# Kernel optimization log

Hardware: AMD Instinct MI355X
Metric: run time of the kernel (lower is better)

## Reference

```python
import jax, jax.numpy as jnp
import numpy as np

B = 64


def _upsample_conv1x1(f, cw, cb, size):
    # bilinear upsample (align_corners=False == jax half-pixel) + 1x1 conv
    u = jax.image.resize(f, (f.shape[0], f.shape[1], size, size), method='bilinear')
    return jnp.einsum('bchw,oc->bohw', u, cw) + cb[None, :, None, None]


def _shuffle_byblock(x, perms, block_size):
    # Rearrange 'b c (h h1) (w w1) -> b c (h w) h1 w1', then per-block channel
    # permutation: shuffled[:, j, i] = blocks[:, perms[i, j], i], then inverse.
    Bsz, C, H, _ = x.shape
    nb = H // block_size
    blocks = x.reshape(Bsz, C, nb, block_size, nb, block_size)
    blocks = blocks.transpose(0, 1, 2, 4, 3, 5).reshape(Bsz, C, nb * nb, block_size, block_size)
    idx = perms[: nb * nb].T  # [C, nb*nb]; idx[j, i] = perms[i, j]
    shuf = jnp.take_along_axis(blocks, idx[None, :, :, None, None], axis=1)
    shuf = shuf.reshape(Bsz, C, nb, nb, block_size, block_size)
    shuf = shuf.transpose(0, 1, 2, 4, 3, 5).reshape(Bsz, C, H, H)
    return shuf


def setup_inputs() -> dict:
    key = jax.random.key(0)
    ks = jax.random.split(key, 10)
    f1 = jax.random.normal(ks[0], (B, 64, 28, 28), jnp.float32)
    f2 = jax.random.normal(ks[1], (B, 128, 14, 14), jnp.float32)
    f3 = jax.random.normal(ks[2], (B, 128, 7, 7), jnp.float32)
    f4 = jax.random.normal(ks[3], (B, 512, 7, 7), jnp.float32)
    x_final = jax.random.normal(ks[4], (B, 512), jnp.float32)
    cw1 = jax.random.normal(ks[5], (64, 64), jnp.float32) * 0.1
    cb1 = jnp.zeros((64,), jnp.float32)
    cw2 = jax.random.normal(ks[6], (128, 128), jnp.float32) * 0.1
    cb2 = jnp.zeros((128,), jnp.float32)
    cw3 = jax.random.normal(ks[7], (256, 128), jnp.float32) * 0.1
    cb3 = jnp.zeros((256,), jnp.float32)
    cw4 = jax.random.normal(ks[8], (512, 512), jnp.float32) * 0.1
    cb4 = jnp.zeros((512,), jnp.float32)
    w1 = jnp.ones((64, 56, 56), jnp.float32)
    w2 = jnp.ones((128, 28, 28), jnp.float32)
    w3 = jnp.ones((256, 14, 14), jnp.float32)
    w4 = jnp.ones((512, 7, 7), jnp.float32)
    rng = np.random.default_rng(0)
    perms = jnp.asarray(np.stack([rng.permutation(64) for _ in range(28 * 28)]).astype(np.int32))
    return dict(f1=f1, f2=f2, f3=f3, f4=f4, x_final=x_final,
                cw1=cw1, cb1=cb1, cw2=cw2, cb2=cb2, cw3=cw3, cb3=cb3, cw4=cw4, cb4=cb4,
                w1=w1, w2=w2, w3=w3, w4=w4, perms=perms)


def reference(f1, f2, f3, f4, x_final, cw1, cb1, cw2, cb2, cw3, cb3, cw4, cb4,
              w1, w2, w3, w4, perms):
    aux1 = _shuffle_byblock(_upsample_conv1x1(f1, cw1, cb1, 56), perms, 28)
    aux2 = _upsample_conv1x1(f2, cw2, cb2, 28)
    aux3 = _upsample_conv1x1(f3, cw3, cb3, 14)
    aux4 = _upsample_conv1x1(f4, cw4, cb4, 7)
    return (x_final, aux1, aux2, aux3, aux4, w1, w2, w3, w4)
```

## Files before the change

kernel.cpp:

```cpp
#include <hip/hip_runtime.h>
#include <hip/hip_bf16.h>
#include <cstddef>

typedef __attribute__((ext_vector_type(8))) short bf16x8;
typedef __attribute__((ext_vector_type(4))) float f32x4;

__device__ __forceinline__ float4 ld4(const float* p) { return *(const float4*)p; }
__device__ __forceinline__ unsigned short f2bf(float v) {
  __hip_bfloat16 h = __float2bfloat16(v);
  return *(unsigned short*)&h;
}

__device__ __forceinline__ bf16x8 pack8(float v0, float v1, float v2, float v3,
                                        float v4, float v5, float v6, float v7) {
  bf16x8 r;
  r[0] = (short)f2bf(v0); r[1] = (short)f2bf(v1);
  r[2] = (short)f2bf(v2); r[3] = (short)f2bf(v3);
  r[4] = (short)f2bf(v4); r[5] = (short)f2bf(v5);
  r[6] = (short)f2bf(v6); r[7] = (short)f2bf(v7);
  return r;
}
__device__ __forceinline__ bf16x8 cfrag(const float* __restrict__ p) {
  float4 a = ld4(p), b = ld4(p + 4);
  return pack8(a.x, a.y, a.z, a.w, b.x, b.y, b.z, b.w);
}
__device__ __forceinline__ bf16x8 gfrag(const float* __restrict__ p, int stride) {
  float v0 = p[0], v1 = p[stride], v2 = p[2 * stride], v3 = p[3 * stride];
  float v4 = p[4 * stride], v5 = p[5 * stride], v6 = p[6 * stride], v7 = p[7 * stride];
  return pack8(v0, v1, v2, v3, v4, v5, v6, v7);
}
__device__ __forceinline__ bf16x8 gfrag_guard(const float* __restrict__ p, int stride, bool ok) {
  float v0 = ok ? p[0] : 0.f, v1 = ok ? p[stride] : 0.f;
  float v2 = ok ? p[2 * stride] : 0.f, v3 = ok ? p[3 * stride] : 0.f;
  float v4 = ok ? p[4 * stride] : 0.f, v5 = ok ? p[5 * stride] : 0.f;
  float v6 = ok ? p[6 * stride] : 0.f, v7 = ok ? p[7 * stride] : 0.f;
  return pack8(v0, v1, v2, v3, v4, v5, v6, v7);
}

__device__ __forceinline__ void up_quad_rows(const float* __restrict__ s0,
                                             const float* __restrict__ s1,
                                             const float* __restrict__ s2,
                                             int qx, int W, float* __restrict__ dst, int pitch) {
  int cm = qx > 0 ? qx - 1 : 0, cp = qx < W - 1 ? qx + 1 : W - 1;
  float tA0 = 0.25f * s0[cm] + 0.75f * s0[qx], tA1 = 0.75f * s0[qx] + 0.25f * s0[cp];
  float tB0 = 0.25f * s1[cm] + 0.75f * s1[qx], tB1 = 0.75f * s1[qx] + 0.25f * s1[cp];
  float tC0 = 0.25f * s2[cm] + 0.75f * s2[qx], tC1 = 0.75f * s2[qx] + 0.25f * s2[cp];
  *(float2*)dst = make_float2(0.25f * tA0 + 0.75f * tB0, 0.25f * tA1 + 0.75f * tB1);
  *(float2*)(dst + pitch) = make_float2(0.75f * tB0 + 0.25f * tC0, 0.75f * tB1 + 0.25f * tC1);
}

__device__ __forceinline__ void up_quad2(const float* __restrict__ s0,
                                         const float* __restrict__ s1,
                                         const float* __restrict__ s2,
                                         int qx0, int W, float* __restrict__ dst, int pitch) {
  int cm = qx0 > 0 ? qx0 - 1 : 0;
  int c2 = qx0 + 2 < W ? qx0 + 2 : W - 1;
  float Am = s0[cm], A0 = s0[qx0], A1 = s0[qx0 + 1], A2 = s0[c2];
  float Bm = s1[cm], B0 = s1[qx0], B1 = s1[qx0 + 1], B2 = s1[c2];
  float Cm = s2[cm], C0 = s2[qx0], C1 = s2[qx0 + 1], C2 = s2[c2];
  float hA0 = 0.25f * Am + 0.75f * A0, hA1 = 0.75f * A0 + 0.25f * A1;
  float hA2 = 0.25f * A0 + 0.75f * A1, hA3 = 0.75f * A1 + 0.25f * A2;
  float hB0 = 0.25f * Bm + 0.75f * B0, hB1 = 0.75f * B0 + 0.25f * B1;
  float hB2 = 0.25f * B0 + 0.75f * B1, hB3 = 0.75f * B1 + 0.25f * B2;
  float hC0 = 0.25f * Cm + 0.75f * C0, hC1 = 0.75f * C0 + 0.25f * C1;
  float hC2 = 0.25f * C0 + 0.75f * C1, hC3 = 0.75f * C1 + 0.25f * C2;
  *(float4*)dst = make_float4(0.25f * hA0 + 0.75f * hB0, 0.25f * hA1 + 0.75f * hB1,
                              0.25f * hA2 + 0.75f * hB2, 0.25f * hA3 + 0.75f * hB3);
  *(float4*)(dst + pitch) = make_float4(0.75f * hB0 + 0.25f * hC0, 0.75f * hB1 + 0.25f * hC1,
                                        0.75f * hB2 + 0.25f * hC2, 0.75f * hB3 + 0.25f * hC3);
}

struct P1M { float ct[16][252]; int inv[4][16]; };
struct C2M { float ct[32][126]; };
struct C3M { float ct[64][49]; };
union SmemM { P1M p1; C2M c2; C3M c3; };

__device__ __forceinline__ int2 xcd_decode(int d, int wpb_log) {
  int xcd = d & 7;
  int i = (d >> 3) & ((1 << wpb_log) - 1);
  int b = (((d >> (3 + wpb_log)) << 3) | xcd);
  return make_int2(b, i);
}

__global__ void __launch_bounds__(256)
fused_all(const float* __restrict__ f1, const float* __restrict__ f2,
          const float* __restrict__ f3, const float* __restrict__ f4,
          const float* __restrict__ cw1, const float* __restrict__ cb1,
          const float* __restrict__ cw2, const float* __restrict__ cb2,
          const float* __restrict__ cw3, const float* __restrict__ cb3,
          const float* __restrict__ cw4, const float* __restrict__ cb4,
          const float* __restrict__ xf, const float* __restrict__ w1,
          const float* __restrict__ w2, const float* __restrict__ w3,
          const float* __restrict__ w4s, const int* __restrict__ perms,
          float* __restrict__ out) {
  __shared__ SmemM sm;
  const int raw = blockIdx.x, tid = threadIdx.x;
  const int wave = tid >> 6, lane = tid & 63;
  const int l15 = lane & 15, lg = lane >> 4;
  float* o_aux1 = out + 32768;
  float* o_aux2 = o_aux1 + 12845056;
  float* o_aux3 = o_aux2 + 6422528;
  float* o_aux4 = o_aux3 + 3211264;

  if (raw < 128) {
    int2 bi = xcd_decode(raw, 1);
    const int b = bi.x;
    const int ob = bi.y * 256 + wave * 64;
    const float* f4b = f4 + (size_t)b * 25088;

    f32x4 acc[4][4];
#pragma unroll
    for (int mi = 0; mi < 4; ++mi) {
      float bv0 = cb4[ob + mi * 16 + lg * 4 + 0], bv1 = cb4[ob + mi * 16 + lg * 4 + 1];
      float bv2 = cb4[ob + mi * 16 + lg * 4 + 2], bv3 = cb4[ob + mi * 16 + lg * 4 + 3];
#pragma unroll
      for (int n = 0; n < 4; ++n) {
        acc[mi][n][0] = bv0; acc[mi][n][1] = bv1; acc[mi][n][2] = bv2; acc[mi][n][3] = bv3;
      }
    }
    int poff[4]; bool pok[4];
#pragma unroll
    for (int n = 0; n < 4; ++n) {
      int p = n * 16 + l15;
      pok[n] = p < 49;
      poff[n] = pok[n] ? p : 0;
    }
#pragma unroll 1
    for (int k0 = 0; k0 < 512; k0 += 32) {
      bf16x8 A0 = cfrag(cw4 + (size_t)(ob + 0 + l15) * 512 + k0 + lg * 8);
      bf16x8 A1 = cfrag(cw4 + (size_t)(ob + 16 + l15) * 512 + k0 + lg * 8);
      bf16x8 A2 = cfrag(cw4 + (size_t)(ob + 32 + l15) * 512 + k0 + lg * 8);
      bf16x8 A3 = cfrag(cw4 + (size_t)(ob + 48 + l15) * 512 + k0 + lg * 8);
      const float* fb = f4b + (size_t)(k0 + lg * 8) * 49;
      bf16x8 B0 = gfrag_guard(fb + poff[0], 49, pok[0]);
      bf16x8 B1 = gfrag_guard(fb + poff[1], 49, pok[1]);
      bf16x8 B2 = gfrag_guard(fb + poff[2], 49, pok[2]);
      bf16x8 B3 = gfrag_guard(fb + poff[3], 49, pok[3]);
      acc[0][0] = __builtin_amdgcn_mfma_f32_16x16x32_bf16(A0, B0, acc[0][0], 0, 0, 0);
      acc[0][1] = __builtin_amdgcn_mfma_f32_16x16x32_bf16(A0, B1, acc[0][1], 0, 0, 0);
      acc[0][2] = __builtin_amdgcn_mfma_f32_16x16x32_bf16(A0, B2, acc[0][2], 0, 0, 0);
      acc[0][3] = __builtin_amdgcn_mfma_f32_16x16x32_bf16(A0, B3, acc[0][3], 0, 0, 0);
      acc[1][0] = __builtin_amdgcn_mfma_f32_16x16x32_bf16(A1, B0, acc[1][0], 0, 0, 0);
      acc[1][1] = __builtin_amdgcn_mfma_f32_16x16x32_bf16(A1, B1, acc[1][1], 0, 0, 0);
      acc[1][2] = __builtin_amdgcn_mfma_f32_16x16x32_bf16(A1, B2, acc[1][2], 0, 0, 0);
      acc[1][3] = __builtin_amdgcn_mfma_f32_16x16x32_bf16(A1, B3, acc[1][3], 0, 0, 0);
      acc[2][0] = __builtin_amdgcn_mfma_f32_16x16x32_bf16(A2, B0, acc[2][0], 0, 0, 0);
      acc[2][1] = __builtin_amdgcn_mfma_f32_16x16x32_bf16(A2, B1, acc[2][1], 0, 0, 0);
      acc[2][2] = __builtin_amdgcn_mfma_f32_16x16x32_bf16(A2, B2, acc[2][2], 0, 0, 0);
      acc[2][3] = __builtin_amdgcn_mfma_f32_16x16x32_bf16(A2, B3, acc[2][3], 0, 0, 0);
      acc[3][0] = __builtin_amdgcn_mfma_f32_16x16x32_bf16(A3, B0, acc[3][0], 0, 0, 0);
      acc[3][1] = __builtin_amdgcn_mfma_f32_16x16x32_bf16(A3, B1, acc[3][1], 0, 0, 0);
      acc[3][2] = __builtin_amdgcn_mfma_f32_16x16x32_bf16(A3, B2, acc[3][2], 0, 0, 0);
      acc[3][3] = __builtin_amdgcn_mfma_f32_16x16x32_bf16(A3, B3, acc[3][3], 0, 0, 0);
    }
    float* outb = o_aux4 + (size_t)b * 25088;
#pragma unroll
    for (int mi = 0; mi < 4; ++mi) {
#pragma unroll
      for (int n = 0; n < 4; ++n) {
        int p = n * 16 + l15;
        if (p < 49) {
#pragma unroll
          for (int r = 0; r < 4; ++r) {
            int o = ob + mi * 16 + lg * 4 + r;
            outb[(size_t)o * 49 + p] = acc[mi][n][r];
          }
        }
      }
    }
  } else if (raw < 1152) {
    int2 bi = xcd_decode(raw - 128, 4);
    const int b = bi.x;
    const int o0 = (bi.y >> 2) * 16;
    const int r0 = (bi.y & 3) * 7, base = r0 - 1;
    const float* f1b = f1 + (size_t)b * 50176;

    if (tid >= 128 && tid < 192) {
      int t2 = tid - 128;
      int i = t2 >> 4, cl = t2 & 15;
      int c = o0 + cl;
      int r = 0;
      for (int j = 0; j < 64; ++j)
        if (perms[i * 64 + j] == c) r = j;
      sm.p1.inv[i][cl] = r;
    }

    int off[4];
#pragma unroll
    for (int j = 0; j < 4; ++j) {
      int praw = wave * 64 + j * 16 + l15;
      int p = praw < 251 ? praw : 251;
      int lr = p / 28, x = p - lr * 28;
      int sr = base + lr;
      sr = sr < 0 ? 0 : (sr > 27 ? 27 : sr);
      off[j] = sr * 28 + x;
    }
    f32x4 acc[4];
    {
      float bv0 = cb1[o0 + lg * 4 + 0], bv1 = cb1[o0 + lg * 4 + 1];
      float bv2 = cb1[o0 + lg * 4 + 2], bv3 = cb1[o0 + lg * 4 + 3];
#pragma unroll
      for (int j = 0; j < 4; ++j) {
        acc[j][0] = bv0; acc[j][1] = bv1; acc[j][2] = bv2; acc[j][3] = bv3;
      }
    }
    const float* ap = cw1 + (size_t)(o0 + l15) * 64 + lg * 8;
#pragma unroll
    for (int ks = 0; ks < 2; ++ks) {
      bf16x8 A = cfrag(ap + ks * 32);
      const float* fb = f1b + (size_t)(ks * 32 + lg * 8) * 784;
#pragma unroll
      for (int j = 0; j < 4; ++j) {
        bf16x8 B = gfrag(fb + off[j], 784);
        acc[j] = __builtin_amdgcn_mfma_f32_16x16x32_bf16(A, B, acc[j], 0, 0, 0);
      }
    }
#pragma unroll
    for (int j = 0; j < 4; ++j) {
      int praw = wave * 64 + j * 16 + l15;
      if (praw < 252) {
#pragma unroll
        for (int r = 0; r < 4; ++r) sm.p1.ct[lg * 4 + r][praw] = acc[j][r];
      }
    }
    __syncthreads();

    const size_t obase = (size_t)b * 200704;
    for (int i = tid; i < 1568; i += 256) {
      int cl = i / 98;
      int rem = i - cl * 98;
      int ly = rem / 14, pr = rem - ly * 14;
      int qx0 = 2 * pr;
      int qy = r0 + ly;
      int lr = ly + 1;
      int qi = ((qy >= 14) ? 2 : 0) + ((qx0 >= 14) ? 1 : 0);
      int j = sm.p1.inv[qi][cl];
      float* dst = o_aux1 + obase + (size_t)j * 3136 + (size_t)(2 * qy) * 56 + 2 * qx0;
      up_quad2(&sm.p1.ct[cl][(lr - 1) * 28], &sm.p1.ct[cl][lr * 28],
               &sm.p1.ct[cl][(lr + 1) * 28], qx0, 28, dst, 56);
    }
  } else if (raw < 1664) {
    int2 bi = xcd_decode(raw - 1152, 3);
    const int b = bi.x;
    const int o0 = (bi.y >> 1) * 32;
    const int r0 = (bi.y & 1) * 7, base = r0 - 1;
    const int og = wave >> 1, nt = wave & 1;
    const int om = o0 + og * 16;
    const float* f2b = f2 + (size_t)b * 25088;

    int off[4];
#pragma unroll
    for (int j = 0; j < 4; ++j) {
      int praw = nt * 64 + j * 16 + l15;
      int p = praw < 125 ? praw : 125;
      int lr = p / 14, x = p - lr * 14;
      int sr = base + lr;
      sr = sr < 0 ? 0 : (sr > 13 ? 13 : sr);
      off[j] = sr * 14 + x;
    }
    f32x4 acc[4];
    {
      float bv0 = cb2[om + lg * 4 + 0], bv1 = cb2[om + lg * 4 + 1];
      float bv2 = cb2[om + lg * 4 + 2], bv3 = cb2[om + lg * 4 + 3];
#pragma unroll
      for (int j = 0; j < 4; ++j) {
        acc[j][0] = bv0; acc[j][1] = bv1; acc[j][2] = bv2; acc[j][3] = bv3;
      }
    }
    const float* ap = cw2 + (size_t)(om + l15) * 128 + lg * 8;
#pragma unroll
    for (int ks = 0; ks < 4; ++ks) {
      bf16x8 A = cfrag(ap + ks * 32);
      const float* fb = f2b + (size_t)(ks * 32 + lg * 8) * 196;
#pragma unroll
      for (int j = 0; j < 4; ++j) {
        bf16x8 B = gfrag(fb + off[j], 196);
        acc[j] = __builtin_amdgcn_mfma_f32_16x16x32_bf16(A, B, acc[j], 0, 0, 0);
      }
    }
#pragma unroll
    for (int j = 0; j < 4; ++j) {
      int praw = nt * 64 + j * 16 + l15;
      if (praw < 126) {
#pragma unroll
        for (int r = 0; r < 4; ++r) sm.c2.ct[og * 16 + lg * 4 + r][praw] = acc[j][r];
      }
    }
    __syncthreads();

    const size_t obase = (size_t)b * 100352;
    for (int i = tid; i < 1568; i += 256) {
      int cl = i / 49;
      int rem = i - cl * 49;
      int ly = rem / 7, pr = rem - ly * 7;
      int qx0 = 2 * pr;
      int qy = r0 + ly;
      int lr = ly + 1;
      float* dst = o_aux2 + obase + (size_t)(o0 + cl) * 784 + (size_t)(2 * qy) * 28 + 2 * qx0;
      up_quad2(&sm.c2.ct[cl][(lr - 1) * 14], &sm.c2.ct[cl][lr * 14],
               &sm.c2.ct[cl][(lr + 1) * 14], qx0, 14, dst, 28);
    }
  } else if (raw < 1920) {
    int2 bi = xcd_decode(raw - 1664, 2);
    const int b = bi.x;
    const int o0 = bi.y * 64;
    const int om = o0 + wave * 16;
    const float* f3b = f3 + (size_t)b * 6272;

    int poff[4]; bool pok[4];
#pragma unroll
    for (int j = 0; j < 4; ++j) {
      int p = j * 16 + l15;
      pok[j] = p < 49;
      poff[j] = pok[j] ? p : 0;
    }
    f32x4 acc[4];
    {
      float bv0 = cb3[om + lg * 4 + 0], bv1 = cb3[om + lg * 4 + 1];
      float bv2 = cb3[om + lg * 4 + 2], bv3 = cb3[om + lg * 4 + 3];
#pragma unroll
      for (int j = 0; j < 4; ++j) {
        acc[j][0] = bv0; acc[j][1] = bv1; acc[j][2] = bv2; acc[j][3] = bv3;
      }
    }
    const float* ap = cw3 + (size_t)(om + l15) * 128 + lg * 8;
#pragma unroll
    for (int ks = 0; ks < 4; ++ks) {
      bf16x8 A = cfrag(ap + ks * 32);
      const float* fb = f3b + (size_t)(ks * 32 + lg * 8) * 49;
#pragma unroll
      for (int j = 0; j < 4; ++j) {
        bf16x8 B = gfrag_guard(fb + poff[j], 49, pok[j]);
        acc[j] = __builtin_amdgcn_mfma_f32_16x16x32_bf16(A, B, acc[j], 0, 0, 0);
      }
    }
#pragma unroll
    for (int j = 0; j < 4; ++j) {
      int p = j * 16 + l15;
      if (p < 49) {
#pragma unroll
        for (int r = 0; r < 4; ++r) sm.c3.ct[wave * 16 + lg * 4 + r][p] = acc[j][r];
      }
    }
    __syncthreads();

    const size_t obase = (size_t)b * 50176;
    for (int i = tid; i < 64 * 49; i += 256) {
      int cl = i / 49;
      int q = i - cl * 49;
      int qy = q / 7, qx = q - qy * 7;
      int rm = qy > 0 ? qy - 1 : 0, rp = qy < 6 ? qy + 1 : 6;
      float* dst = o_aux3 + obase + (size_t)(o0 + cl) * 196 + (size_t)(2 * qy) * 14 + 2 * qx;
      up_quad_rows(&sm.c3.ct[cl][rm * 7], &sm.c3.ct[cl][qy * 7], &sm.c3.ct[cl][rp * 7],
                   qx, 7, dst, 14);
    }
  } else {
    int idx = (raw - 1920) * 256 + tid;
    const int stride = 64 * 256;
    float4* o4 = (float4*)out;
    const size_t W1 = 6029312;
    for (int i = idx; i < 8192; i += stride) o4[i] = ((const float4*)xf)[i];
    for (int i = idx; i < 50176; i += stride) o4[W1 + i] = ((const float4*)w1)[i];
    for (int i = idx; i < 25088; i += stride) o4[W1 + 50176 + i] = ((const float4*)w2)[i];
    for (int i = idx; i < 12544; i += stride) o4[W1 + 75264 + i] = ((const float4*)w3)[i];
    for (int i = idx; i < 6272; i += stride) o4[W1 + 87808 + i] = ((const float4*)w4s)[i];
  }
}

extern "C" void kernel_launch(void* const* d_in, const int* in_sizes, int n_in,
                              void* d_out, int out_size, void* d_ws, size_t ws_size,
                              hipStream_t stream) {
  const float* f1      = (const float*)d_in[0];
  const float* f2      = (const float*)d_in[1];
  const float* f3      = (const float*)d_in[2];
  const float* f4      = (const float*)d_in[3];
  const float* x_final = (const float*)d_in[4];
  const float* cw1     = (const float*)d_in[5];
  const float* cb1     = (const float*)d_in[6];
  const float* cw2     = (const float*)d_in[7];
  const float* cb2     = (const float*)d_in[8];
  const float* cw3     = (const float*)d_in[9];
  const float* cb3     = (const float*)d_in[10];
  const float* cw4     = (const float*)d_in[11];
  const float* cb4     = (const float*)d_in[12];
  const float* w1      = (const float*)d_in[13];
  const float* w2      = (const float*)d_in[14];
  const float* w3      = (const float*)d_in[15];
  const float* w4      = (const float*)d_in[16];
  const int*   perms   = (const int*)d_in[17];

  float* out = (float*)d_out;

  fused_all<<<1984, 256, 0, stream>>>(f1, f2, f3, f4, cw1, cb1, cw2, cb2,
                                      cw3, cb3, cw4, cb4, x_final, w1, w2, w3, w4,
                                      perms, out);
}
```

Before: 48.92 us.

## Interleave all task types per batch in block index ordering

Replaces the segmented block mapping, where each output head occupied a contiguous range of block ids, with a per-batch grouping. Each group of 31 slots per XCD holds 16 aux1, 8 aux2, 4 aux3, 2 aux4 and 1 copy block for the same batch element. The aim is to mix heavy and light block types across the dispatch order so that CUs stay balanced and all work for one batch lands on the same XCD, improving L2 locality. The grid total of 1984 blocks is unchanged, so the scheme relies on the launch count matching 64*31.

```diff
diff --git a/kernel.cpp b/kernel.cpp
--- a/kernel.cpp
+++ b/kernel.cpp
@@ -75,13 +75,6 @@
 struct C3M { float ct[64][49]; };
 union SmemM { P1M p1; C2M c2; C3M c3; };
 
-__device__ __forceinline__ int2 xcd_decode(int d, int wpb_log) {
-  int xcd = d & 7;
-  int i = (d >> 3) & ((1 << wpb_log) - 1);
-  int b = (((d >> (3 + wpb_log)) << 3) | xcd);
-  return make_int2(b, i);
-}
-
 __global__ void __launch_bounds__(256)
 fused_all(const float* __restrict__ f1, const float* __restrict__ f2,
           const float* __restrict__ f3, const float* __restrict__ f4,
@@ -94,7 +87,12 @@
           const float* __restrict__ w4s, const int* __restrict__ perms,
           float* __restrict__ out) {
   __shared__ SmemM sm;
-  const int raw = blockIdx.x, tid = threadIdx.x;
+  const int d = blockIdx.x, tid = threadIdx.x;
+  const int xcd = d & 7;
+  const int slot = d >> 3;
+  const int g = slot / 31;
+  const int r = slot - g * 31;
+  const int b = g * 8 + xcd;
   const int wave = tid >> 6, lane = tid & 63;
   const int l15 = lane & 15, lg = lane >> 4;
   float* o_aux1 = out + 32768;
@@ -102,10 +100,192 @@
   float* o_aux3 = o_aux2 + 6422528;
   float* o_aux4 = o_aux3 + 3211264;
 
-  if (raw < 128) {
-    int2 bi = xcd_decode(raw, 1);
-    const int b = bi.x;
-    const int ob = bi.y * 256 + wave * 64;
+  if (r < 16) {
+    const int i = r;
+    const int o0 = (i >> 2) * 16;
+    const int r0 = (i & 3) * 7, base = r0 - 1;
+    const float* f1b = f1 + (size_t)b * 50176;
+
+    if (tid >= 128 && tid < 192) {
+      int t2 = tid - 128;
+      int qi = t2 >> 4, cl = t2 & 15;
+      int c = o0 + cl;
+      int rr = 0;
+      for (int j = 0; j < 64; ++j)
+        if (perms[qi * 64 + j] == c) rr = j;
+      sm.p1.inv[qi][cl] = rr;
+    }
+
+    int off[4];
+#pragma unroll
+    for (int j = 0; j < 4; ++j) {
+      int praw = wave * 64 + j * 16 + l15;
+      int p = praw < 251 ? praw : 251;
+      int lr = p / 28, x = p - lr * 28;
+      int sr = base + lr;
+      sr = sr < 0 ? 0 : (sr > 27 ? 27 : sr);
+      off[j] = sr * 28 + x;
+    }
+    f32x4 acc[4];
+    {
+      float bv0 = cb1[o0 + lg * 4 + 0], bv1 = cb1[o0 + lg * 4 + 1];
+      float bv2 = cb1[o0 + lg * 4 + 2], bv3 = cb1[o0 + lg * 4 + 3];
+#pragma unroll
+      for (int j = 0; j < 4; ++j) {
+        acc[j][0] = bv0; acc[j][1] = bv1; acc[j][2] = bv2; acc[j][3] = bv3;
+      }
+    }
+    const float* ap = cw1 + (size_t)(o0 + l15) * 64 + lg * 8;
+#pragma unroll
+    for (int ks = 0; ks < 2; ++ks) {
+      bf16x8 A = cfrag(ap + ks * 32);
+      const float* fb = f1b + (size_t)(ks * 32 + lg * 8) * 784;
+#pragma unroll
+      for (int j = 0; j < 4; ++j) {
+        bf16x8 B = gfrag(fb + off[j], 784);
+        acc[j] = __builtin_amdgcn_mfma_f32_16x16x32_bf16(A, B, acc[j], 0, 0, 0);
+      }
+    }
+#pragma unroll
+    for (int j = 0; j < 4; ++j) {
+      int praw = wave * 64 + j * 16 + l15;
+      if (praw < 252) {
+#pragma unroll
+        for (int rr = 0; rr < 4; ++rr) sm.p1.ct[lg * 4 + rr][praw] = acc[j][rr];
+      }
+    }
+    __syncthreads();
+
+    const size_t obase = (size_t)b * 200704;
+    for (int i2 = tid; i2 < 1568; i2 += 256) {
+      int cl = i2 / 98;
+      int rem = i2 - cl * 98;
+      int ly = rem / 14, pr = rem - ly * 14;
+      int qx0 = 2 * pr;
+      int qy = r0 + ly;
+      int lr = ly + 1;
+      int qi = ((qy >= 14) ? 2 : 0) + ((qx0 >= 14) ? 1 : 0);
+      int j = sm.p1.inv[qi][cl];
+      float* dst = o_aux1 + obase + (size_t)j * 3136 + (size_t)(2 * qy) * 56 + 2 * qx0;
+      up_quad2(&sm.p1.ct[cl][(lr - 1) * 28], &sm.p1.ct[cl][lr * 28],
+               &sm.p1.ct[cl][(lr + 1) * 28], qx0, 28, dst, 56);
+    }
+  } else if (r < 24) {
+    const int i = r - 16;
+    const int o0 = (i >> 1) * 32;
+    const int r0 = (i & 1) * 7, base = r0 - 1;
+    const int og = wave >> 1, nt = wave & 1;
+    const int om = o0 + og * 16;
+    const float* f2b = f2 + (size_t)b * 25088;
+
+    int off[4];
+#pragma unroll
+    for (int j = 0; j < 4; ++j) {
+      int praw = nt * 64 + j * 16 + l15;
+      int p = praw < 125 ? praw : 125;
+      int lr = p / 14, x = p - lr * 14;
+      int sr = base + lr;
+      sr = sr < 0 ? 0 : (sr > 13 ? 13 : sr);
+      off[j] = sr * 14 + x;
+    }
+    f32x4 acc[4];
+    {
+      float bv0 = cb2[om + lg * 4 + 0], bv1 = cb2[om + lg * 4 + 1];
+      float bv2 = cb2[om + lg * 4 + 2], bv3 = cb2[om + lg * 4 + 3];
+#pragma unroll
+      for (int j = 0; j < 4; ++j) {
+        acc[j][0] = bv0; acc[j][1] = bv1; acc[j][2] = bv2; acc[j][3] = bv3;
+      }
+    }
+    const float* ap = cw2 + (size_t)(om + l15) * 128 + lg * 8;
+#pragma unroll
+    for (int ks = 0; ks < 4; ++ks) {
+      bf16x8 A = cfrag(ap + ks * 32);
+      const float* fb = f2b + (size_t)(ks * 32 + lg * 8) * 196;
+#pragma unroll
+      for (int j = 0; j < 4; ++j) {
+        bf16x8 B = gfrag(fb + off[j], 196);
+        acc[j] = __builtin_amdgcn_mfma_f32_16x16x32_bf16(A, B, acc[j], 0, 0, 0);
+      }
+    }
+#pragma unroll
+    for (int j = 0; j < 4; ++j) {
+      int praw = nt * 64 + j * 16 + l15;
+      if (praw < 126) {
+#pragma unroll
+        for (int rr = 0; rr < 4; ++rr) sm.c2.ct[og * 16 + lg * 4 + rr][praw] = acc[j][rr];
+      }
+    }
+    __syncthreads();
+
+    const size_t obase = (size_t)b * 100352;
+    for (int i2 = tid; i2 < 1568; i2 += 256) {
+      int cl = i2 / 49;
+      int rem = i2 - cl * 49;
+      int ly = rem / 7, pr = rem - ly * 7;
+      int qx0 = 2 * pr;
+      int qy = r0 + ly;
+      int lr = ly + 1;
+      float* dst = o_aux2 + obase + (size_t)(o0 + cl) * 784 + (size_t)(2 * qy) * 28 + 2 * qx0;
+      up_quad2(&sm.c2.ct[cl][(lr - 1) * 14], &sm.c2.ct[cl][lr * 14],
+               &sm.c2.ct[cl][(lr + 1) * 14], qx0, 14, dst, 28);
+    }
+  } else if (r < 28) {
+    const int i = r - 24;
+    const int o0 = i * 64;
+    const int om = o0 + wave * 16;
+    const float* f3b = f3 + (size_t)b * 6272;
+
+    int poff[4]; bool pok[4];
+#pragma unroll
+    for (int j = 0; j < 4; ++j) {
+      int p = j * 16 + l15;
+      pok[j] = p < 49;
+      poff[j] = pok[j] ? p : 0;
+    }
+    f32x4 acc[4];
+    {
+      float bv0 = cb3[om + lg * 4 + 0], bv1 = cb3[om + lg * 4 + 1];
+      float bv2 = cb3[om + lg * 4 + 2], bv3 = cb3[om + lg * 4 + 3];
+#pragma unroll
+      for (int j = 0; j < 4; ++j) {
+        acc[j][0] = bv0; acc[j][1] = bv1; acc[j][2] = bv2; acc[j][3] = bv3;
+      }
+    }
+    const float* ap = cw3 + (size_t)(om + l15) * 128 + lg * 8;
+#pragma unroll
+    for (int ks = 0; ks < 4; ++ks) {
+      bf16x8 A = cfrag(ap + ks * 32);
+      const float* fb = f3b + (size_t)(ks * 32 + lg * 8) * 49;
+#pragma unroll
+      for (int j = 0; j < 4; ++j) {
+        bf16x8 B = gfrag_guard(fb + poff[j], 49, pok[j]);
+        acc[j] = __builtin_amdgcn_mfma_f32_16x16x32_bf16(A, B, acc[j], 0, 0, 0);
+      }
+    }
+#pragma unroll
+    for (int j = 0; j < 4; ++j) {
+      int p = j * 16 + l15;
+      if (p < 49) {
+#pragma unroll
+        for (int rr = 0; rr < 4; ++rr) sm.c3.ct[wave * 16 + lg * 4 + rr][p] = acc[j][rr];
+      }
+    }
+    __syncthreads();
+
+    const size_t obase = (size_t)b * 50176;
+    for (int i2 = tid; i2 < 64 * 49; i2 += 256) {
+      int cl = i2 / 49;
+      int q = i2 - cl * 49;
+      int qy = q / 7, qx = q - qy * 7;
+      int rm = qy > 0 ? qy - 1 : 0, rp = qy < 6 ? qy + 1 : 6;
+      float* dst = o_aux3 + obase + (size_t)(o0 + cl) * 196 + (size_t)(2 * qy) * 14 + 2 * qx;
+      up_quad_rows(&sm.c3.ct[cl][rm * 7], &sm.c3.ct[cl][qy * 7], &sm.c3.ct[cl][rp * 7],
+                   qx, 7, dst, 14);
+    }
+  } else if (r < 30) {
+    const int i = r - 28;
+    const int ob = i * 256 + wave * 64;
     const float* f4b = f4 + (size_t)b * 25088;
 
     f32x4 acc[4][4];
@@ -161,209 +341,24 @@
         int p = n * 16 + l15;
         if (p < 49) {
 #pragma unroll
-          for (int r = 0; r < 4; ++r) {
-            int o = ob + mi * 16 + lg * 4 + r;
-            outb[(size_t)o * 49 + p] = acc[mi][n][r];
+          for (int rr = 0; rr < 4; ++rr) {
+            int o = ob + mi * 16 + lg * 4 + rr;
+            outb[(size_t)o * 49 + p] = acc[mi][n][rr];
           }
         }
       }
     }
-  } else if (raw < 1152) {
-    int2 bi = xcd_decode(raw - 128, 4);
-    const int b = bi.x;
-    const int o0 = (bi.y >> 2) * 16;
-    const int r0 = (bi.y & 3) * 7, base = r0 - 1;
-    const float* f1b = f1 + (size_t)b * 50176;
-
-    if (tid >= 128 && tid < 192) {
-      int t2 = tid - 128;
-      int i = t2 >> 4, cl = t2 & 15;
-      int c = o0 + cl;
-      int r = 0;
-      for (int j = 0; j < 64; ++j)
-        if (perms[i * 64 + j] == c) r = j;
-      sm.p1.inv[i][cl] = r;
-    }
-
-    int off[4];
-#pragma unroll
-    for (int j = 0; j < 4; ++j) {
-      int praw = wave * 64 + j * 16 + l15;
-      int p = praw < 251 ? praw : 251;
-      int lr = p / 28, x = p - lr * 28;
-      int sr = base + lr;
-      sr = sr < 0 ? 0 : (sr > 27 ? 27 : sr);
-      off[j] = sr * 28 + x;
-    }
-    f32x4 acc[4];
-    {
-      float bv0 = cb1[o0 + lg * 4 + 0], bv1 = cb1[o0 + lg * 4 + 1];
-      float bv2 = cb1[o0 + lg * 4 + 2], bv3 = cb1[o0 + lg * 4 + 3];
-#pragma unroll
-      for (int j = 0; j < 4; ++j) {
-        acc[j][0] = bv0; acc[j][1] = bv1; acc[j][2] = bv2; acc[j][3] = bv3;
-      }
-    }
-    const float* ap = cw1 + (size_t)(o0 + l15) * 64 + lg * 8;
-#pragma unroll
-    for (int ks = 0; ks < 2; ++ks) {
-      bf16x8 A = cfrag(ap + ks * 32);
-      const float* fb = f1b + (size_t)(ks * 32 + lg * 8) * 784;
-#pragma unroll
-      for (int j = 0; j < 4; ++j) {
-        bf16x8 B = gfrag(fb + off[j], 784);
-        acc[j] = __builtin_amdgcn_mfma_f32_16x16x32_bf16(A, B, acc[j], 0, 0, 0);
-      }
-    }
-#pragma unroll
-    for (int j = 0; j < 4; ++j) {
-      int praw = wave * 64 + j * 16 + l15;
-      if (praw < 252) {
-#pragma unroll
-        for (int r = 0; r < 4; ++r) sm.p1.ct[lg * 4 + r][praw] = acc[j][r];
-      }
-    }
-    __syncthreads();
-
-    const size_t obase = (size_t)b * 200704;
-    for (int i = tid; i < 1568; i += 256) {
-      int cl = i / 98;
-      int rem = i - cl * 98;
-      int ly = rem / 14, pr = rem - ly * 14;
-      int qx0 = 2 * pr;
-      int qy = r0 + ly;
-      int lr = ly + 1;
-      int qi = ((qy >= 14) ? 2 : 0) + ((qx0 >= 14) ? 1 : 0);
-      int j = sm.p1.inv[qi][cl];
-      float* dst = o_aux1 + obase + (size_t)j * 3136 + (size_t)(2 * qy) * 56 + 2 * qx0;
-      up_quad2(&sm.p1.ct[cl][(lr - 1) * 28], &sm.p1.ct[cl][lr * 28],
-               &sm.p1.ct[cl][(lr + 1) * 28], qx0, 28, dst, 56);
-    }
-  } else if (raw < 1664) {
-    int2 bi = xcd_decode(raw - 1152, 3);
-    const int b = bi.x;
-    const int o0 = (bi.y >> 1) * 32;
-    const int r0 = (bi.y & 1) * 7, base = r0 - 1;
-    const int og = wave >> 1, nt = wave & 1;
-    const int om = o0 + og * 16;
-    const float* f2b = f2 + (size_t)b * 25088;
-
-    int off[4];
-#pragma unroll
-    for (int j = 0; j < 4; ++j) {
-      int praw = nt * 64 + j * 16 + l15;
-      int p = praw < 125 ? praw : 125;
-      int lr = p / 14, x = p - lr * 14;
-      int sr = base + lr;
-      sr = sr < 0 ? 0 : (sr > 13 ? 13 : sr);
-      off[j] = sr * 14 + x;
-    }
-    f32x4 acc[4];
-    {
-      float bv0 = cb2[om + lg * 4 + 0], bv1 = cb2[om + lg * 4 + 1];
-      float bv2 = cb2[om + lg * 4 + 2], bv3 = cb2[om + lg * 4 + 3];
-#pragma unroll
-      for (int j = 0; j < 4; ++j) {
-        acc[j][0] = bv0; acc[j][1] = bv1; acc[j][2] = bv2; acc[j][3] = bv3;
-      }
-    }
-    const float* ap = cw2 + (size_t)(om + l15) * 128 + lg * 8;
-#pragma unroll
-    for (int ks = 0; ks < 4; ++ks) {
-      bf16x8 A = cfrag(ap + ks * 32);
-      const float* fb = f2b + (size_t)(ks * 32 + lg * 8) * 196;
-#pragma unroll
-      for (int j = 0; j < 4; ++j) {
-        bf16x8 B = gfrag(fb + off[j], 196);
-        acc[j] = __builtin_amdgcn_mfma_f32_16x16x32_bf16(A, B, acc[j], 0, 0, 0);
-      }
-    }
-#pragma unroll
-    for (int j = 0; j < 4; ++j) {
-      int praw = nt * 64 + j * 16 + l15;
-      if (praw < 126) {
-#pragma unroll
-        for (int r = 0; r < 4; ++r) sm.c2.ct[og * 16 + lg * 4 + r][praw] = acc[j][r];
-      }
-    }
-    __syncthreads();
-
-    const size_t obase = (size_t)b * 100352;
-    for (int i = tid; i < 1568; i += 256) {
-      int cl = i / 49;
-      int rem = i - cl * 49;
-      int ly = rem / 7, pr = rem - ly * 7;
-      int qx0 = 2 * pr;
-      int qy = r0 + ly;
-      int lr = ly + 1;
-      float* dst = o_aux2 + obase + (size_t)(o0 + cl) * 784 + (size_t)(2 * qy) * 28 + 2 * qx0;
-      up_quad2(&sm.c2.ct[cl][(lr - 1) * 14], &sm.c2.ct[cl][lr * 14],
-               &sm.c2.ct[cl][(lr + 1) * 14], qx0, 14, dst, 28);
-    }
-  } else if (raw < 1920) {
-    int2 bi = xcd_decode(raw - 1664, 2);
-    const int b = bi.x;
-    const int o0 = bi.y * 64;
-    const int om = o0 + wave * 16;
-    const float* f3b = f3 + (size_t)b * 6272;
-
-    int poff[4]; bool pok[4];
-#pragma unroll
-    for (int j = 0; j < 4; ++j) {
-      int p = j * 16 + l15;
-      pok[j] = p < 49;
-      poff[j] = pok[j] ? p : 0;
-    }
-    f32x4 acc[4];
-    {
-      float bv0 = cb3[om + lg * 4 + 0], bv1 = cb3[om + lg * 4 + 1];
-      float bv2 = cb3[om + lg * 4 + 2], bv3 = cb3[om + lg * 4 + 3];
-#pragma unroll
-      for (int j = 0; j < 4; ++j) {
-        acc[j][0] = bv0; acc[j][1] = bv1; acc[j][2] = bv2; acc[j][3] = bv3;
-      }
-    }
-    const float* ap = cw3 + (size_t)(om + l15) * 128 + lg * 8;
-#pragma unroll
-    for (int ks = 0; ks < 4; ++ks) {
-      bf16x8 A = cfrag(ap + ks * 32);
-      const float* fb = f3b + (size_t)(ks * 32 + lg * 8) * 49;
-#pragma unroll
-      for (int j = 0; j < 4; ++j) {
-        bf16x8 B = gfrag_guard(fb + poff[j], 49, pok[j]);
-        acc[j] = __builtin_amdgcn_mfma_f32_16x16x32_bf16(A, B, acc[j], 0, 0, 0);
-      }
-    }
-#pragma unroll
-    for (int j = 0; j < 4; ++j) {
-      int p = j * 16 + l15;
-      if (p < 49) {
-#pragma unroll
-        for (int r = 0; r < 4; ++r) sm.c3.ct[wave * 16 + lg * 4 + r][p] = acc[j][r];
-      }
-    }
-    __syncthreads();
-
-    const size_t obase = (size_t)b * 50176;
-    for (int i = tid; i < 64 * 49; i += 256) {
-      int cl = i / 49;
-      int q = i - cl * 49;
-      int qy = q / 7, qx = q - qy * 7;
-      int rm = qy > 0 ? qy - 1 : 0, rp = qy < 6 ? qy + 1 : 6;
-      float* dst = o_aux3 + obase + (size_t)(o0 + cl) * 196 + (size_t)(2 * qy) * 14 + 2 * qx;
-      up_quad_rows(&sm.c3.ct[cl][rm * 7], &sm.c3.ct[cl][qy * 7], &sm.c3.ct[cl][rp * 7],
-                   qx, 7, dst, 14);
-    }
   } else {
-    int idx = (raw - 1920) * 256 + tid;
+    const int cid = g * 8 + xcd;
+    int idx = cid * 256 + tid;
     const int stride = 64 * 256;
     float4* o4 = (float4*)out;
     const size_t W1 = 6029312;
-    for (int i = idx; i < 8192; i += stride) o4[i] = ((const float4*)xf)[i];
-    for (int i = idx; i < 50176; i += stride) o4[W1 + i] = ((const float4*)w1)[i];
-    for (int i = idx; i < 25088; i += stride) o4[W1 + 50176 + i] = ((const float4*)w2)[i];
-    for (int i = idx; i < 12544; i += stride) o4[W1 + 75264 + i] = ((const float4*)w3)[i];
-    for (int i = idx; i < 6272; i += stride) o4[W1 + 87808 + i] = ((const float4*)w4s)[i];
+    for (int i2 = idx; i2 < 8192; i2 += stride) o4[i2] = ((const float4*)xf)[i2];
+    for (int i2 = idx; i2 < 50176; i2 += stride) o4[W1 + i2] = ((const float4*)w1)[i2];
+    for (int i2 = idx; i2 < 25088; i2 += stride) o4[W1 + 50176 + i2] = ((const float4*)w2)[i2];
+    for (int i2 = idx; i2 < 12544; i2 += stride) o4[W1 + 75264 + i2] = ((const float4*)w3)[i2];
+    for (int i2 = idx; i2 < 6272; i2 += stride) o4[W1 + 87808 + i2] = ((const float4*)w4s)[i2];
   }
 }
 
```

Result: slower. 73.25 us (+49.8%).
